# Optimization experiments

Hardware: AMD Instinct MI355X
Metric: run time of the kernel (lower is better)

Reference implementation:

```python
import jax, jax.numpy as jnp
import numpy as np

N = 100000      # nodes
E = 1600000     # edges (avg degree 16)
NFEAT = 256
HIDDEN = 256
C = 4           # channels
PC = HIDDEN // C  # per-channel dim = 64
NCLASS = 4
EPS = 1e-12


def setup_inputs() -> dict:
    key = jax.random.key(0)
    ks = jax.random.split(key, 12)
    x = jax.random.normal(ks[0], (N, NFEAT), dtype=jnp.float32)
    row = jax.random.randint(ks[1], (E,), 0, N, dtype=jnp.int64)
    col = jax.random.randint(ks[2], (E,), 0, N, dtype=jnp.int64)
    s = lambda fan_in: 1.0 / np.sqrt(fan_in)
    # NeiborAssigner: Linear(2*nfeat, C) -> Linear(C, C)
    asg_W1 = jax.random.normal(ks[3], (C, 2 * NFEAT), dtype=jnp.float32) * s(2 * NFEAT)
    asg_b1 = jnp.zeros((C,), dtype=jnp.float32)
    asg_W2 = jax.random.normal(ks[4], (C, C), dtype=jnp.float32) * s(C)
    asg_b2 = jnp.zeros((C,), dtype=jnp.float32)
    # DisenLayer: per-channel Linear(nfeat, PC) and conv Linear(PC, PC, bias=False)
    lin_W = jax.random.normal(ks[5], (C, PC, NFEAT), dtype=jnp.float32) * s(NFEAT)
    lin_b = jax.random.normal(ks[6], (C, PC), dtype=jnp.float32) * 0.01
    conv_W = jax.random.normal(ks[7], (C, PC, PC), dtype=jnp.float32) * s(PC)
    bias = jax.random.normal(ks[8], (C, PC), dtype=jnp.float32) * 0.01
    # classifier Linear(hidden, nclass)
    cls_W = jax.random.normal(ks[9], (NCLASS, HIDDEN), dtype=jnp.float32) * s(HIDDEN)
    cls_b = jnp.zeros((NCLASS,), dtype=jnp.float32)
    return {"x": x, "row": row, "col": col,
            "asg_W1": asg_W1, "asg_b1": asg_b1, "asg_W2": asg_W2, "asg_b2": asg_b2,
            "lin_W": lin_W, "lin_b": lin_b, "conv_W": conv_W, "bias": bias,
            "cls_W": cls_W, "cls_b": cls_b}


def reference(x, row, col, asg_W1, asg_b1, asg_W2, asg_b2,
              lin_W, lin_b, conv_W, bias, cls_W, cls_b):
    # --- NeiborAssigner on detached features ---
    xd = jax.lax.stop_gradient(x)
    # cat([x[col], x[row]]) @ W1.T  ==  x[col]@W1a.T + x[row]@W1b.T  (project per node first)
    W1a, W1b = asg_W1[:, :NFEAT], asg_W1[:, NFEAT:]
    proj_a = xd @ W1a.T          # [N, C]
    proj_b = xd @ W1b.T          # [N, C]
    h1 = proj_a[col] + proj_b[row] + asg_b1       # [E, C]
    h2 = h1 @ asg_W2.T + asg_b2                    # [E, C]
    edge_weight = jax.nn.softmax(h2, axis=1)       # [E, C]

    # --- DisenLayer (single layer, layer_num=2) ---
    # per-channel reduce:  z_k = lin_k(x);  c_k = z_k @ conv_W_k.T
    z = jnp.einsum('nf,kpf->nkp', x, lin_W) + lin_b[None]   # [N, C, PC]
    c = jnp.einsum('nkp,kqp->nkq', z, conv_W)               # [N, C, PC]
    # weighted sparse propagate: out[row] += edge_weight[:,k] * c[col]
    msg = c[col] * edge_weight[:, :, None]                  # [E, C, PC]
    out = jax.ops.segment_sum(msg, row, num_segments=N)     # [N, C, PC]
    out = out + bias[None]                                  # per-channel bias
    # F.normalize(p=2, dim=1) per channel
    nrm = jnp.sqrt(jnp.sum(out * out, axis=-1, keepdims=True))
    out = out / jnp.maximum(nrm, EPS)
    h = out.reshape(N, HIDDEN)                              # channel concat
    # dropout is identity in eval mode

    # --- classifier ---
    logits = h @ cls_W.T + cls_b                            # [N, nclass]
    return (h, logits)
```

## Files before the change

kernel.cpp:

```cpp
#include <hip/hip_runtime.h>
#include <hip/hip_bf16.h>

#define N_NODES 100000
#define N_EDGES 1600000
#define BCAP    64
#define EPS     1e-12f

typedef __bf16 bf16x8 __attribute__((ext_vector_type(8)));
typedef float  f32x4  __attribute__((ext_vector_type(4)));

__device__ __forceinline__ unsigned short f2bf(float f){
    union { float f; unsigned int i; } v; v.f = f;
    unsigned int x = v.i;
    return (unsigned short)((x + 0x7fffu + ((x >> 16) & 1u)) >> 16);
}
__device__ __forceinline__ float bits2f(unsigned int u){
    union { unsigned int i; float f; } v; v.i = u; return v.f;
}

__global__ void k_init(int* __restrict__ deg,
                       const float* __restrict__ lin_W,
                       const float* __restrict__ lin_b,
                       const float* __restrict__ conv_W,
                       __bf16* __restrict__ Mbf,
                       float* __restrict__ dvec,
                       const float* __restrict__ asg_W1,
                       __bf16* __restrict__ W1bf){
    int b = blockIdx.x;
    int t = threadIdx.x;
    if (b < 391){
        int i = b * 256 + t;
        if (i < N_NODES) deg[i] = 0;
    } else if (b < 647){
        int id = (b - 391) * 256 + t;
        int f  = id & 255;
        int o  = id >> 8;
        int k  = o >> 6;
        const float* cw = conv_W + o * 64;
        const float* lw = lin_W + k * 64 * 256 + f;
        float s = 0.f;
        #pragma unroll 8
        for (int p = 0; p < 64; ++p) s += cw[p] * lw[p * 256];
        Mbf[id] = (__bf16)s;
        if (f == 0){
            const float* lb = lin_b + k * 64;
            float d = 0.f;
            for (int p = 0; p < 64; ++p) d += lb[p] * cw[p];
            dvec[o] = d;
        }
    } else {
        int id = (b - 647) * 256 + t;
        int f  = id & 255;
        int o  = id >> 8;
        float v = 0.f;
        if (o < 4)      v = asg_W1[o * 512 + f];
        else if (o < 8) v = asg_W1[(o - 4) * 512 + 256 + f];
        W1bf[id] = (__bf16)v;
    }
}

__global__ __launch_bounds__(256) void k_gemm(const float* __restrict__ x,
                                              const __bf16* __restrict__ Mbf,
                                              const __bf16* __restrict__ W1bf,
                                              const float* __restrict__ dvec,
                                              __bf16* __restrict__ c,
                                              float* __restrict__ proj_a,
                                              float* __restrict__ proj_b){
    int lane = threadIdx.x & 63, wv = threadIdx.x >> 6;
    int wm = wv & 1, wn = wv >> 1;
    int nb = blockIdx.x * 64 + wm * 32;
    int ob = wn * 128;
    int l15 = lane & 15, quad = lane >> 4;
    f32x4 acc[2][8], accp[2];
    #pragma unroll
    for (int mi = 0; mi < 2; ++mi){
        accp[mi] = f32x4{0.f, 0.f, 0.f, 0.f};
        #pragma unroll
        for (int ni = 0; ni < 8; ++ni) acc[mi][ni] = f32x4{0.f, 0.f, 0.f, 0.f};
    }
    const float* xg[2];
    #pragma unroll
    for (int mi = 0; mi < 2; ++mi){
        int row = nb + mi * 16 + l15;
        if (row >= N_NODES) row = N_NODES - 1;
        xg[mi] = x + (size_t)row * 256 + quad * 8;
    }
    for (int k0 = 0; k0 < 256; k0 += 32){
        bf16x8 a[2];
        #pragma unroll
        for (int mi = 0; mi < 2; ++mi){
            float4 lo = *(const float4*)(xg[mi] + k0);
            float4 hi = *(const float4*)(xg[mi] + k0 + 4);
            a[mi][0] = (__bf16)lo.x; a[mi][1] = (__bf16)lo.y;
            a[mi][2] = (__bf16)lo.z; a[mi][3] = (__bf16)lo.w;
            a[mi][4] = (__bf16)hi.x; a[mi][5] = (__bf16)hi.y;
            a[mi][6] = (__bf16)hi.z; a[mi][7] = (__bf16)hi.w;
        }
        #pragma unroll
        for (int ni = 0; ni < 8; ++ni){
            bf16x8 b = *(const bf16x8*)(Mbf + (size_t)(ob + ni * 16 + l15) * 256 + k0 + quad * 8);
            acc[0][ni] = __builtin_amdgcn_mfma_f32_16x16x32_bf16(a[0], b, acc[0][ni], 0, 0, 0);
            acc[1][ni] = __builtin_amdgcn_mfma_f32_16x16x32_bf16(a[1], b, acc[1][ni], 0, 0, 0);
        }
        if (wn == 0){
            bf16x8 bw = *(const bf16x8*)(W1bf + (size_t)l15 * 256 + k0 + quad * 8);
            accp[0] = __builtin_amdgcn_mfma_f32_16x16x32_bf16(a[0], bw, accp[0], 0, 0, 0);
            accp[1] = __builtin_amdgcn_mfma_f32_16x16x32_bf16(a[1], bw, accp[1], 0, 0, 0);
        }
    }
    #pragma unroll
    for (int ni = 0; ni < 8; ++ni){
        int o = ob + ni * 16 + l15;
        float dv = dvec[o];
        #pragma unroll
        for (int mi = 0; mi < 2; ++mi){
            int nrow = nb + mi * 16 + quad * 4;
            #pragma unroll
            for (int r = 0; r < 4; ++r){
                int node = nrow + r;
                if (node < N_NODES) c[(size_t)node * 256 + o] = (__bf16)(acc[mi][ni][r] + dv);
            }
        }
    }
    if (wn == 0 && l15 < 8){
        #pragma unroll
        for (int mi = 0; mi < 2; ++mi){
            int nrow = nb + mi * 16 + quad * 4;
            #pragma unroll
            for (int r = 0; r < 4; ++r){
                int node = nrow + r;
                if (node < N_NODES){
                    float v = accp[mi][r];
                    if (l15 < 4) proj_a[node * 4 + l15] = v;
                    else         proj_b[node * 4 + (l15 - 4)] = v;
                }
            }
        }
    }
}

__global__ __launch_bounds__(256) void k_edge(const void* __restrict__ row_raw,
                                              const void* __restrict__ col_raw,
                                              const float* __restrict__ proj_a,
                                              const float* __restrict__ proj_b,
                                              const float* __restrict__ asg_b1,
                                              const float* __restrict__ asg_W2,
                                              const float* __restrict__ asg_b2,
                                              int* __restrict__ deg,
                                              int4* __restrict__ bucket){
    __shared__ int s_is64;
    int t = threadIdx.x;
    if (t == 0) s_is64 = 1;
    __syncthreads();
    unsigned v = ((const unsigned*)row_raw)[2 * t + 1] | ((const unsigned*)col_raw)[2 * t + 1];
    if (v) s_is64 = 0;
    __syncthreads();

    int e = blockIdx.x * 256 + t;
    if (e >= N_EDGES) return;
    int r, cl;
    if (s_is64){
        r  = (int)((const long long*)row_raw)[e];
        cl = (int)((const long long*)col_raw)[e];
    } else {
        r  = ((const int*)row_raw)[e];
        cl = ((const int*)col_raw)[e];
    }
    float4 pa = *(const float4*)(proj_a + (size_t)cl * 4);
    float4 pb = *(const float4*)(proj_b + (size_t)r * 4);
    float h1[4];
    h1[0] = pa.x + pb.x + asg_b1[0];
    h1[1] = pa.y + pb.y + asg_b1[1];
    h1[2] = pa.z + pb.z + asg_b1[2];
    h1[3] = pa.w + pb.w + asg_b1[3];
    float h2[4];
    #pragma unroll
    for (int i = 0; i < 4; ++i){
        float s = asg_b2[i];
        #pragma unroll
        for (int j = 0; j < 4; ++j) s += asg_W2[i * 4 + j] * h1[j];
        h2[i] = s;
    }
    float m = fmaxf(fmaxf(h2[0], h2[1]), fmaxf(h2[2], h2[3]));
    float e0 = __expf(h2[0] - m), e1 = __expf(h2[1] - m);
    float e2 = __expf(h2[2] - m), e3 = __expf(h2[3] - m);
    float inv = 1.f / (e0 + e1 + e2 + e3);
    unsigned b0 = f2bf(e0 * inv), b1 = f2bf(e1 * inv);
    unsigned b2 = f2bf(e2 * inv), b3 = f2bf(e3 * inv);
    int4 rec;
    rec.x = cl;
    rec.y = (int)(b0 | (b1 << 16));
    rec.z = (int)(b2 | (b3 << 16));
    rec.w = 0;
    int pos = atomicAdd(&deg[r], 1);
    if (pos < BCAP) bucket[(size_t)r * BCAP + pos] = rec;
}

__global__ __launch_bounds__(256) void k_node(const __bf16* __restrict__ c,
                                              const int* __restrict__ deg,
                                              const int4* __restrict__ bucket,
                                              const float* __restrict__ bias,
                                              const float* __restrict__ cls_W,
                                              const float* __restrict__ cls_b,
                                              float* __restrict__ out_h,
                                              float* __restrict__ out_logits){
    int wv = __builtin_amdgcn_readfirstlane((int)(threadIdx.x >> 6));
    int l  = threadIdx.x & 63;
    int n  = blockIdx.x * 4 + wv;
    int k2 = l >> 4;

    float4 bi = *(const float4*)(bias  + l * 4);
    float4 w0 = *(const float4*)(cls_W + 0 * 256 + l * 4);
    float4 w1 = *(const float4*)(cls_W + 1 * 256 + l * 4);
    float4 w2 = *(const float4*)(cls_W + 2 * 256 + l * 4);
    float4 w3 = *(const float4*)(cls_W + 3 * 256 + l * 4);

    int dn = deg[n]; if (dn > BCAP) dn = BCAP;
    const int4* rec = bucket + (size_t)n * BCAP;
    const __bf16* cb = c + (size_t)l * 4;

    bool hi2 = (k2 & 2) != 0;
    bool odd = (k2 & 1) != 0;

    float a0 = 0.f, a1 = 0.f, a2 = 0.f, a3 = 0.f;
    #pragma unroll 4
    for (int i = 0; i < dn; ++i){
        int4 rc = rec[i];
        int  ww = hi2 ? rc.z : rc.y;
        unsigned wb = odd ? ((unsigned)ww & 0xffff0000u) : ((unsigned)ww << 16);
        float w = bits2f(wb);
        uint2 vv = *(const uint2*)(cb + (size_t)rc.x * 256);
        a0 += w * bits2f(vv.x << 16);
        a1 += w * bits2f(vv.x & 0xffff0000u);
        a2 += w * bits2f(vv.y << 16);
        a3 += w * bits2f(vv.y & 0xffff0000u);
    }
    a0 += bi.x; a1 += bi.y; a2 += bi.z; a3 += bi.w;

    float ss = a0 * a0 + a1 * a1 + a2 * a2 + a3 * a3;
    ss += __shfl_xor(ss, 1);
    ss += __shfl_xor(ss, 2);
    ss += __shfl_xor(ss, 4);
    ss += __shfl_xor(ss, 8);
    float nrm = fmaxf(sqrtf(ss), EPS);
    float h0 = a0 / nrm, h1 = a1 / nrm, h2 = a2 / nrm, h3 = a3 / nrm;
    *(float4*)(out_h + (size_t)n * 256 + l * 4) = make_float4(h0, h1, h2, h3);

    float p0 = h0 * w0.x + h1 * w0.y + h2 * w0.z + h3 * w0.w;
    float p1 = h0 * w1.x + h1 * w1.y + h2 * w1.z + h3 * w1.w;
    float p2 = h0 * w2.x + h1 * w2.y + h2 * w2.z + h3 * w2.w;
    float p3 = h0 * w3.x + h1 * w3.y + h2 * w3.z + h3 * w3.w;
    #pragma unroll
    for (int off = 1; off < 64; off <<= 1){
        p0 += __shfl_xor(p0, off);
        p1 += __shfl_xor(p1, off);
        p2 += __shfl_xor(p2, off);
        p3 += __shfl_xor(p3, off);
    }
    if (l == 0){
        float4 lg = make_float4(p0 + cls_b[0], p1 + cls_b[1],
                                p2 + cls_b[2], p3 + cls_b[3]);
        *(float4*)(out_logits + (size_t)n * 4) = lg;
    }
}

extern "C" void kernel_launch(void* const* d_in, const int* in_sizes, int n_in,
                              void* d_out, int out_size, void* d_ws, size_t ws_size,
                              hipStream_t stream){
    const float* x       = (const float*)d_in[0];
    const void*  row_raw = d_in[1];
    const void*  col_raw = d_in[2];
    const float* asg_W1  = (const float*)d_in[3];
    const float* asg_b1  = (const float*)d_in[4];
    const float* asg_W2  = (const float*)d_in[5];
    const float* asg_b2  = (const float*)d_in[6];
    const float* lin_W   = (const float*)d_in[7];
    const float* lin_b   = (const float*)d_in[8];
    const float* conv_W  = (const float*)d_in[9];
    const float* bias    = (const float*)d_in[10];
    const float* cls_W   = (const float*)d_in[11];
    const float* cls_b   = (const float*)d_in[12];

    char* ws = (char*)d_ws;
    size_t off = 0;
    auto alloc = [&](size_t bytes) -> void* {
        void* p = ws + off;
        off += (bytes + 255) & ~(size_t)255;
        return p;
    };
    __bf16* c      = (__bf16*)alloc((size_t)N_NODES * 256 * 2);
    int4*   bucket = (int4*)alloc((size_t)N_NODES * BCAP * 16);
    float*  proj_a = (float*)alloc((size_t)N_NODES * 4 * 4);
    float*  proj_b = (float*)alloc((size_t)N_NODES * 4 * 4);
    __bf16* Mbf    = (__bf16*)alloc(65536 * 2);
    __bf16* W1bf   = (__bf16*)alloc(4096 * 2);
    float*  dvec   = (float*)alloc(256 * 4);
    int*    deg    = (int*)alloc((size_t)N_NODES * 4);

    float* out_h = (float*)d_out;
    float* out_l = out_h + (size_t)N_NODES * 256;

    hipLaunchKernelGGL(k_init, dim3(663), dim3(256), 0, stream,
                       deg, lin_W, lin_b, conv_W, Mbf, dvec, asg_W1, W1bf);
    hipLaunchKernelGGL(k_gemm, dim3((N_NODES + 63) / 64), dim3(256), 0, stream,
                       x, (const __bf16*)Mbf, (const __bf16*)W1bf, dvec, c, proj_a, proj_b);
    hipLaunchKernelGGL(k_edge, dim3(N_EDGES / 256), dim3(256), 0, stream,
                       row_raw, col_raw, proj_a, proj_b, asg_b1, asg_W2, asg_b2,
                       deg, bucket);
    hipLaunchKernelGGL(k_node, dim3(N_NODES / 4), dim3(256), 0, stream,
                       c, deg, bucket, bias, cls_W, cls_b, out_h, out_l);
}
```

Baseline: 500.6 us.

## Retile node GEMM to 32-row blocks with register prefetch of x

The GEMM kernel now gives each block 32 nodes, with each of the four waves owning 64 output columns instead of a 2x2 wave split over 64 nodes. This halves the accumulator registers per wave, and a minimum-occupancy launch bound is added. The next k-slice of x is loaded into registers before the current MFMAs run, so load latency can overlap with compute. In exchange, each x row is now read by all four waves instead of two, and there are twice as many blocks.

```diff
diff --git a/kernel.cpp b/kernel.cpp
--- a/kernel.cpp
+++ b/kernel.cpp
@@ -59,7 +59,7 @@
     }
 }
 
-__global__ __launch_bounds__(256) void k_gemm(const float* __restrict__ x,
+__global__ __launch_bounds__(256, 4) void k_gemm(const float* __restrict__ x,
                                               const __bf16* __restrict__ Mbf,
                                               const __bf16* __restrict__ W1bf,
                                               const float* __restrict__ dvec,
@@ -67,16 +67,15 @@
                                               float* __restrict__ proj_a,
                                               float* __restrict__ proj_b){
     int lane = threadIdx.x & 63, wv = threadIdx.x >> 6;
-    int wm = wv & 1, wn = wv >> 1;
-    int nb = blockIdx.x * 64 + wm * 32;
-    int ob = wn * 128;
+    int nb = blockIdx.x * 32;
+    int ob = wv * 64;
     int l15 = lane & 15, quad = lane >> 4;
-    f32x4 acc[2][8], accp[2];
+    f32x4 acc[2][4], accp[2];
     #pragma unroll
     for (int mi = 0; mi < 2; ++mi){
         accp[mi] = f32x4{0.f, 0.f, 0.f, 0.f};
         #pragma unroll
-        for (int ni = 0; ni < 8; ++ni) acc[mi][ni] = f32x4{0.f, 0.f, 0.f, 0.f};
+        for (int ni = 0; ni < 4; ++ni) acc[mi][ni] = f32x4{0.f, 0.f, 0.f, 0.f};
     }
     const float* xg[2];
     #pragma unroll
@@ -85,31 +84,48 @@
         if (row >= N_NODES) row = N_NODES - 1;
         xg[mi] = x + (size_t)row * 256 + quad * 8;
     }
+    float4 cl[2], ch[2];
+    #pragma unroll
+    for (int mi = 0; mi < 2; ++mi){
+        cl[mi] = *(const float4*)(xg[mi]);
+        ch[mi] = *(const float4*)(xg[mi] + 4);
+    }
     for (int k0 = 0; k0 < 256; k0 += 32){
+        float4 nl[2], nh[2];
+        bool pf = (k0 < 224);
+        if (pf){
+            #pragma unroll
+            for (int mi = 0; mi < 2; ++mi){
+                nl[mi] = *(const float4*)(xg[mi] + k0 + 32);
+                nh[mi] = *(const float4*)(xg[mi] + k0 + 36);
+            }
+        }
         bf16x8 a[2];
         #pragma unroll
         for (int mi = 0; mi < 2; ++mi){
-            float4 lo = *(const float4*)(xg[mi] + k0);
-            float4 hi = *(const float4*)(xg[mi] + k0 + 4);
-            a[mi][0] = (__bf16)lo.x; a[mi][1] = (__bf16)lo.y;
-            a[mi][2] = (__bf16)lo.z; a[mi][3] = (__bf16)lo.w;
-            a[mi][4] = (__bf16)hi.x; a[mi][5] = (__bf16)hi.y;
-            a[mi][6] = (__bf16)hi.z; a[mi][7] = (__bf16)hi.w;
-        }
-        #pragma unroll
-        for (int ni = 0; ni < 8; ++ni){
+            a[mi][0] = (__bf16)cl[mi].x; a[mi][1] = (__bf16)cl[mi].y;
+            a[mi][2] = (__bf16)cl[mi].z; a[mi][3] = (__bf16)cl[mi].w;
+            a[mi][4] = (__bf16)ch[mi].x; a[mi][5] = (__bf16)ch[mi].y;
+            a[mi][6] = (__bf16)ch[mi].z; a[mi][7] = (__bf16)ch[mi].w;
+        }
+        #pragma unroll
+        for (int ni = 0; ni < 4; ++ni){
             bf16x8 b = *(const bf16x8*)(Mbf + (size_t)(ob + ni * 16 + l15) * 256 + k0 + quad * 8);
             acc[0][ni] = __builtin_amdgcn_mfma_f32_16x16x32_bf16(a[0], b, acc[0][ni], 0, 0, 0);
             acc[1][ni] = __builtin_amdgcn_mfma_f32_16x16x32_bf16(a[1], b, acc[1][ni], 0, 0, 0);
         }
-        if (wn == 0){
+        if (wv == 0){
             bf16x8 bw = *(const bf16x8*)(W1bf + (size_t)l15 * 256 + k0 + quad * 8);
             accp[0] = __builtin_amdgcn_mfma_f32_16x16x32_bf16(a[0], bw, accp[0], 0, 0, 0);
             accp[1] = __builtin_amdgcn_mfma_f32_16x16x32_bf16(a[1], bw, accp[1], 0, 0, 0);
         }
-    }
-    #pragma unroll
-    for (int ni = 0; ni < 8; ++ni){
+        if (pf){
+            #pragma unroll
+            for (int mi = 0; mi < 2; ++mi){ cl[mi] = nl[mi]; ch[mi] = nh[mi]; }
+        }
+    }
+    #pragma unroll
+    for (int ni = 0; ni < 4; ++ni){
         int o = ob + ni * 16 + l15;
         float dv = dvec[o];
         #pragma unroll
@@ -122,7 +138,7 @@
             }
         }
     }
-    if (wn == 0 && l15 < 8){
+    if (wv == 0 && l15 < 8){
         #pragma unroll
         for (int mi = 0; mi < 2; ++mi){
             int nrow = nb + mi * 16 + quad * 4;
@@ -302,7 +318,7 @@
 
     hipLaunchKernelGGL(k_init, dim3(663), dim3(256), 0, stream,
                        deg, lin_W, lin_b, conv_W, Mbf, dvec, asg_W1, W1bf);
-    hipLaunchKernelGGL(k_gemm, dim3((N_NODES + 63) / 64), dim3(256), 0, stream,
+    hipLaunchKernelGGL(k_gemm, dim3((N_NODES + 31) / 32), dim3(256), 0, stream,
                        x, (const __bf16*)Mbf, (const __bf16*)W1bf, dvec, c, proj_a, proj_b);
     hipLaunchKernelGGL(k_edge, dim3(N_EDGES / 256), dim3(256), 0, stream,
                        row_raw, col_raw, proj_a, proj_b, asg_b1, asg_W2, asg_b2,
```

Result: slower. 515.7 us (+3.0%).

## Split projection into own kernel and co-schedule main GEMM with edge pass

Applied to the files above, without the earlier changes.

The small assigner projection (proj_a/proj_b) now runs in a separate lightweight kernel. The large per-channel GEMM that produces c is merged with the edge-softmax/bucketing kernel, interleaving one GEMM block per four edge blocks. The aim is to overlap compute-bound MFMA work with latency-bound scattered gathers and atomics, and to drop a kernel boundary. In exchange x is read twice and the projection gets its own launch, and register pressure in the merged kernel may limit occupancy.

```diff
diff --git a/kernel.cpp b/kernel.cpp
--- a/kernel.cpp
+++ b/kernel.cpp
@@ -59,25 +59,16 @@
     }
 }
 
-__global__ __launch_bounds__(256) void k_gemm(const float* __restrict__ x,
-                                              const __bf16* __restrict__ Mbf,
-                                              const __bf16* __restrict__ W1bf,
-                                              const float* __restrict__ dvec,
-                                              __bf16* __restrict__ c,
-                                              float* __restrict__ proj_a,
-                                              float* __restrict__ proj_b){
+__global__ __launch_bounds__(256, 4) void k_proj(const float* __restrict__ x,
+                                                 const __bf16* __restrict__ W1bf,
+                                                 float* __restrict__ proj_a,
+                                                 float* __restrict__ proj_b){
     int lane = threadIdx.x & 63, wv = threadIdx.x >> 6;
-    int wm = wv & 1, wn = wv >> 1;
-    int nb = blockIdx.x * 64 + wm * 32;
-    int ob = wn * 128;
+    int nb = blockIdx.x * 128 + wv * 32;
     int l15 = lane & 15, quad = lane >> 4;
-    f32x4 acc[2][8], accp[2];
-    #pragma unroll
-    for (int mi = 0; mi < 2; ++mi){
-        accp[mi] = f32x4{0.f, 0.f, 0.f, 0.f};
-        #pragma unroll
-        for (int ni = 0; ni < 8; ++ni) acc[mi][ni] = f32x4{0.f, 0.f, 0.f, 0.f};
-    }
+    f32x4 accp[2];
+    accp[0] = f32x4{0.f, 0.f, 0.f, 0.f};
+    accp[1] = f32x4{0.f, 0.f, 0.f, 0.f};
     const float* xg[2];
     #pragma unroll
     for (int mi = 0; mi < 2; ++mi){
@@ -96,33 +87,11 @@
             a[mi][4] = (__bf16)hi.x; a[mi][5] = (__bf16)hi.y;
             a[mi][6] = (__bf16)hi.z; a[mi][7] = (__bf16)hi.w;
         }
-        #pragma unroll
-        for (int ni = 0; ni < 8; ++ni){
-            bf16x8 b = *(const bf16x8*)(Mbf + (size_t)(ob + ni * 16 + l15) * 256 + k0 + quad * 8);
-            acc[0][ni] = __builtin_amdgcn_mfma_f32_16x16x32_bf16(a[0], b, acc[0][ni], 0, 0, 0);
-            acc[1][ni] = __builtin_amdgcn_mfma_f32_16x16x32_bf16(a[1], b, acc[1][ni], 0, 0, 0);
-        }
-        if (wn == 0){
-            bf16x8 bw = *(const bf16x8*)(W1bf + (size_t)l15 * 256 + k0 + quad * 8);
-            accp[0] = __builtin_amdgcn_mfma_f32_16x16x32_bf16(a[0], bw, accp[0], 0, 0, 0);
-            accp[1] = __builtin_amdgcn_mfma_f32_16x16x32_bf16(a[1], bw, accp[1], 0, 0, 0);
-        }
-    }
-    #pragma unroll
-    for (int ni = 0; ni < 8; ++ni){
-        int o = ob + ni * 16 + l15;
-        float dv = dvec[o];
-        #pragma unroll
-        for (int mi = 0; mi < 2; ++mi){
-            int nrow = nb + mi * 16 + quad * 4;
-            #pragma unroll
-            for (int r = 0; r < 4; ++r){
-                int node = nrow + r;
-                if (node < N_NODES) c[(size_t)node * 256 + o] = (__bf16)(acc[mi][ni][r] + dv);
-            }
-        }
-    }
-    if (wn == 0 && l15 < 8){
+        bf16x8 bw = *(const bf16x8*)(W1bf + (size_t)l15 * 256 + k0 + quad * 8);
+        accp[0] = __builtin_amdgcn_mfma_f32_16x16x32_bf16(a[0], bw, accp[0], 0, 0, 0);
+        accp[1] = __builtin_amdgcn_mfma_f32_16x16x32_bf16(a[1], bw, accp[1], 0, 0, 0);
+    }
+    if (l15 < 8){
         #pragma unroll
         for (int mi = 0; mi < 2; ++mi){
             int nrow = nb + mi * 16 + quad * 4;
@@ -139,61 +108,120 @@
     }
 }
 
-__global__ __launch_bounds__(256) void k_edge(const void* __restrict__ row_raw,
-                                              const void* __restrict__ col_raw,
-                                              const float* __restrict__ proj_a,
-                                              const float* __restrict__ proj_b,
-                                              const float* __restrict__ asg_b1,
-                                              const float* __restrict__ asg_W2,
-                                              const float* __restrict__ asg_b2,
-                                              int* __restrict__ deg,
-                                              int4* __restrict__ bucket){
+__global__ __launch_bounds__(256, 3) void k_ge(const float* __restrict__ x,
+                                               const __bf16* __restrict__ Mbf,
+                                               const float* __restrict__ dvec,
+                                               __bf16* __restrict__ c,
+                                               const void* __restrict__ row_raw,
+                                               const void* __restrict__ col_raw,
+                                               const float* __restrict__ proj_a,
+                                               const float* __restrict__ proj_b,
+                                               const float* __restrict__ asg_b1,
+                                               const float* __restrict__ asg_W2,
+                                               const float* __restrict__ asg_b2,
+                                               int* __restrict__ deg,
+                                               int4* __restrict__ bucket){
     __shared__ int s_is64;
+    int b = blockIdx.x;
     int t = threadIdx.x;
-    if (t == 0) s_is64 = 1;
-    __syncthreads();
-    unsigned v = ((const unsigned*)row_raw)[2 * t + 1] | ((const unsigned*)col_raw)[2 * t + 1];
-    if (v) s_is64 = 0;
-    __syncthreads();
-
-    int e = blockIdx.x * 256 + t;
-    if (e >= N_EDGES) return;
-    int r, cl;
-    if (s_is64){
-        r  = (int)((const long long*)row_raw)[e];
-        cl = (int)((const long long*)col_raw)[e];
+    if (b % 5 == 0){
+        int gid = b / 5;
+        int lane = t & 63, wv = t >> 6;
+        int wm = wv & 1, wn = wv >> 1;
+        int nb = gid * 64 + wm * 32;
+        int ob = wn * 128;
+        int l15 = lane & 15, quad = lane >> 4;
+        f32x4 acc[2][8];
+        #pragma unroll
+        for (int mi = 0; mi < 2; ++mi)
+            #pragma unroll
+            for (int ni = 0; ni < 8; ++ni) acc[mi][ni] = f32x4{0.f, 0.f, 0.f, 0.f};
+        const float* xg[2];
+        #pragma unroll
+        for (int mi = 0; mi < 2; ++mi){
+            int row = nb + mi * 16 + l15;
+            if (row >= N_NODES) row = N_NODES - 1;
+            xg[mi] = x + (size_t)row * 256 + quad * 8;
+        }
+        for (int k0 = 0; k0 < 256; k0 += 32){
+            bf16x8 a[2];
+            #pragma unroll
+            for (int mi = 0; mi < 2; ++mi){
+                float4 lo = *(const float4*)(xg[mi] + k0);
+                float4 hi = *(const float4*)(xg[mi] + k0 + 4);
+                a[mi][0] = (__bf16)lo.x; a[mi][1] = (__bf16)lo.y;
+                a[mi][2] = (__bf16)lo.z; a[mi][3] = (__bf16)lo.w;
+                a[mi][4] = (__bf16)hi.x; a[mi][5] = (__bf16)hi.y;
+                a[mi][6] = (__bf16)hi.z; a[mi][7] = (__bf16)hi.w;
+            }
+            #pragma unroll
+            for (int ni = 0; ni < 8; ++ni){
+                bf16x8 bb = *(const bf16x8*)(Mbf + (size_t)(ob + ni * 16 + l15) * 256 + k0 + quad * 8);
+                acc[0][ni] = __builtin_amdgcn_mfma_f32_16x16x32_bf16(a[0], bb, acc[0][ni], 0, 0, 0);
+                acc[1][ni] = __builtin_amdgcn_mfma_f32_16x16x32_bf16(a[1], bb, acc[1][ni], 0, 0, 0);
+            }
+        }
+        #pragma unroll
+        for (int ni = 0; ni < 8; ++ni){
+            int o = ob + ni * 16 + l15;
+            float dv = dvec[o];
+            #pragma unroll
+            for (int mi = 0; mi < 2; ++mi){
+                int nrow = nb + mi * 16 + quad * 4;
+                #pragma unroll
+                for (int r = 0; r < 4; ++r){
+                    int node = nrow + r;
+                    if (node < N_NODES) c[(size_t)node * 256 + o] = (__bf16)(acc[mi][ni][r] + dv);
+                }
+            }
+        }
     } else {
-        r  = ((const int*)row_raw)[e];
-        cl = ((const int*)col_raw)[e];
-    }
-    float4 pa = *(const float4*)(proj_a + (size_t)cl * 4);
-    float4 pb = *(const float4*)(proj_b + (size_t)r * 4);
-    float h1[4];
-    h1[0] = pa.x + pb.x + asg_b1[0];
-    h1[1] = pa.y + pb.y + asg_b1[1];
-    h1[2] = pa.z + pb.z + asg_b1[2];
-    h1[3] = pa.w + pb.w + asg_b1[3];
-    float h2[4];
-    #pragma unroll
-    for (int i = 0; i < 4; ++i){
-        float s = asg_b2[i];
-        #pragma unroll
-        for (int j = 0; j < 4; ++j) s += asg_W2[i * 4 + j] * h1[j];
-        h2[i] = s;
-    }
-    float m = fmaxf(fmaxf(h2[0], h2[1]), fmaxf(h2[2], h2[3]));
-    float e0 = __expf(h2[0] - m), e1 = __expf(h2[1] - m);
-    float e2 = __expf(h2[2] - m), e3 = __expf(h2[3] - m);
-    float inv = 1.f / (e0 + e1 + e2 + e3);
-    unsigned b0 = f2bf(e0 * inv), b1 = f2bf(e1 * inv);
-    unsigned b2 = f2bf(e2 * inv), b3 = f2bf(e3 * inv);
-    int4 rec;
-    rec.x = cl;
-    rec.y = (int)(b0 | (b1 << 16));
-    rec.z = (int)(b2 | (b3 << 16));
-    rec.w = 0;
-    int pos = atomicAdd(&deg[r], 1);
-    if (pos < BCAP) bucket[(size_t)r * BCAP + pos] = rec;
+        int eid = b - b / 5 - 1;
+        if (t == 0) s_is64 = 1;
+        __syncthreads();
+        unsigned v = ((const unsigned*)row_raw)[2 * t + 1] | ((const unsigned*)col_raw)[2 * t + 1];
+        if (v) s_is64 = 0;
+        __syncthreads();
+
+        int e = eid * 256 + t;
+        if (e >= N_EDGES) return;
+        int r, cl;
+        if (s_is64){
+            r  = (int)((const long long*)row_raw)[e];
+            cl = (int)((const long long*)col_raw)[e];
+        } else {
+            r  = ((const int*)row_raw)[e];
+            cl = ((const int*)col_raw)[e];
+        }
+        float4 pa = *(const float4*)(proj_a + (size_t)cl * 4);
+        float4 pb = *(const float4*)(proj_b + (size_t)r * 4);
+        float h1[4];
+        h1[0] = pa.x + pb.x + asg_b1[0];
+        h1[1] = pa.y + pb.y + asg_b1[1];
+        h1[2] = pa.z + pb.z + asg_b1[2];
+        h1[3] = pa.w + pb.w + asg_b1[3];
+        float h2[4];
+        #pragma unroll
+        for (int i = 0; i < 4; ++i){
+            float s = asg_b2[i];
+            #pragma unroll
+            for (int j = 0; j < 4; ++j) s += asg_W2[i * 4 + j] * h1[j];
+            h2[i] = s;
+        }
+        float m = fmaxf(fmaxf(h2[0], h2[1]), fmaxf(h2[2], h2[3]));
+        float e0 = __expf(h2[0] - m), e1 = __expf(h2[1] - m);
+        float e2 = __expf(h2[2] - m), e3 = __expf(h2[3] - m);
+        float inv = 1.f / (e0 + e1 + e2 + e3);
+        unsigned b0 = f2bf(e0 * inv), b1 = f2bf(e1 * inv);
+        unsigned b2 = f2bf(e2 * inv), b3 = f2bf(e3 * inv);
+        int4 rec;
+        rec.x = cl;
+        rec.y = (int)(b0 | (b1 << 16));
+        rec.z = (int)(b2 | (b3 << 16));
+        rec.w = 0;
+        int pos = atomicAdd(&deg[r], 1);
+        if (pos < BCAP) bucket[(size_t)r * BCAP + pos] = rec;
+    }
 }
 
 __global__ __launch_bounds__(256) void k_node(const __bf16* __restrict__ c,
@@ -302,9 +330,10 @@
 
     hipLaunchKernelGGL(k_init, dim3(663), dim3(256), 0, stream,
                        deg, lin_W, lin_b, conv_W, Mbf, dvec, asg_W1, W1bf);
-    hipLaunchKernelGGL(k_gemm, dim3((N_NODES + 63) / 64), dim3(256), 0, stream,
-                       x, (const __bf16*)Mbf, (const __bf16*)W1bf, dvec, c, proj_a, proj_b);
-    hipLaunchKernelGGL(k_edge, dim3(N_EDGES / 256), dim3(256), 0, stream,
+    hipLaunchKernelGGL(k_proj, dim3((N_NODES + 127) / 128), dim3(256), 0, stream,
+                       x, (const __bf16*)W1bf, proj_a, proj_b);
+    hipLaunchKernelGGL(k_ge, dim3(7813), dim3(256), 0, stream,
+                       x, (const __bf16*)Mbf, dvec, c,
                        row_raw, col_raw, proj_a, proj_b, asg_b1, asg_W2, asg_b2,
                        deg, bucket);
     hipLaunchKernelGGL(k_node, dim3(N_NODES / 4), dim3(256), 0, stream,
```

Result: no change. 500.3 us (-0.0%).
